# Kernel tuning notes

Hardware: AMD Instinct MI355X
Metric: run time of the kernel (lower is better)

The kernel has to match this reference:

```python
import jax, jax.numpy as jnp
import numpy as np

B, T, E, H, L, V = 16, 512, 512, 8, 4, 2048
HS = E // H  # head_size = n_embd // n_head
FF = 4 * E


def _ln(x, g, b):
    m = x.mean(-1, keepdims=True)
    v = ((x - m) ** 2).mean(-1, keepdims=True)
    return (x - m) * jax.lax.rsqrt(v + 1e-5) * g + b


def setup_inputs() -> dict:
    key = jax.random.key(0)
    ks = jax.random.split(key, 16)
    s = jnp.float32(0.02)
    return {
        "idx": jax.random.randint(ks[0], (B, T), 0, V),
        "tok_emb": jax.random.normal(ks[1], (V, E), jnp.float32) * s,
        "pos_emb": jax.random.normal(ks[2], (T, E), jnp.float32) * s,
        "Wq": jax.random.normal(ks[3], (L, E, E), jnp.float32) * s,
        "Wk": jax.random.normal(ks[4], (L, E, E), jnp.float32) * s,
        "Wv": jax.random.normal(ks[5], (L, E, E), jnp.float32) * s,
        "rel": jax.random.normal(ks[6], (L, 2 * T - 1, HS), jnp.float32) * s,
        "Wo": jax.random.normal(ks[7], (L, E, E), jnp.float32) * s,
        "bo": jnp.zeros((L, E), jnp.float32),
        "ln1_g": jnp.ones((L, E), jnp.float32),
        "ln1_b": jnp.zeros((L, E), jnp.float32),
        "W1": jax.random.normal(ks[8], (L, E, FF), jnp.float32) * s,
        "b1": jnp.zeros((L, FF), jnp.float32),
        "W2": jax.random.normal(ks[9], (L, FF, E), jnp.float32) * s,
        "b2": jnp.zeros((L, E), jnp.float32),
        "ln2_g": jnp.ones((L, E), jnp.float32),
        "ln2_b": jnp.zeros((L, E), jnp.float32),
        "lnf_g": jnp.ones((E,), jnp.float32),
        "lnf_b": jnp.zeros((E,), jnp.float32),
        "Wlm": jax.random.normal(ks[10], (E, V), jnp.float32) * s,
        "blm": jnp.zeros((V,), jnp.float32),
    }


def reference(idx, tok_emb, pos_emb, Wq, Wk, Wv, rel, Wo, bo, ln1_g, ln1_b,
              W1, b1, W2, b2, ln2_g, ln2_b, lnf_g, lnf_b, Wlm, blm):
    x = tok_emb[idx] + pos_emb[None, :T]  # (B,T,E)
    ri = jnp.arange(T)
    rel_idx = ri[:, None] - ri[None, :] + (T - 1)  # block_size == T
    causal = ri[:, None] >= ri[None, :]            # (T,T) lower-triangular
    scale = jnp.float32(1.0 / np.sqrt(HS))
    for l in range(L):
        h = _ln(x, ln1_g[l], ln1_b[l])
        # NOTE: torch code does .view(B, H, T, HS) on a (B, T, H*HS) tensor
        # (NOT a transpose) -- jnp.reshape matches row-major view semantics.
        q = (h @ Wq[l]).reshape(B, H, T, HS)
        k = (h @ Wk[l]).reshape(B, H, T, HS)
        v = (h @ Wv[l]).reshape(B, H, T, HS)
        re = rel[l][rel_idx]  # (T,T,HS)
        # rel scores: sum_d q[b,h,i,d]*re[i,j,d]; avoid the 5D intermediate
        scores = jnp.einsum('bhid,bhjd->bhij', q, k) * scale \
               + jnp.einsum('bhid,ijd->bhij', q, re)
        scores = jnp.where(causal, scores, -jnp.inf)
        att = jax.nn.softmax(scores, axis=-1)  # dropout disabled (eval)
        ctx = jnp.einsum('bhij,bhjd->bhid', att, v)
        ctx = jnp.swapaxes(ctx, 1, 2).reshape(B, T, H * HS)
        x = x + ctx @ Wo[l] + bo[l]
        h2 = _ln(x, ln2_g[l], ln2_b[l])
        x = x + jax.nn.relu(h2 @ W1[l] + b1[l]) @ W2[l] + b2[l]
    x = _ln(x, lnf_g, lnf_b)
    return x @ Wlm + blm  # logits (B,T,V)
```

## Files before the change

kernel.cpp:

```cpp
#include <hip/hip_runtime.h>
#include <hip/hip_bf16.h>
#include <stdint.h>

typedef __hip_bfloat16 bf16;
typedef __attribute__((ext_vector_type(8))) short bf16x8;
typedef __attribute__((ext_vector_type(8))) short short8;
typedef __attribute__((ext_vector_type(4))) float f32x4;

#define DEV __device__ __forceinline__

static constexpr int Bn = 16, Tn = 512, En = 512, Hn = 8, Ln = 4, Vn = 2048;
static constexpr int HSn = 64, FFn = 2048, Mn = Bn * Tn;
static constexpr int SQ = 1536;

DEV f32x4 mfma16(bf16x8 a, bf16x8 b, f32x4 c) {
  return __builtin_amdgcn_mfma_f32_16x16x32_bf16(a, b, c, 0, 0, 0);
}
DEV float b2f(bf16 x) { return __bfloat162float(x); }
DEV bf16 f2b(float x) { return __float2bfloat16(x); }
DEV short f2s(float x) { bf16 h = f2b(x); return reinterpret_cast<short&>(h); }

DEV void gload16(const void* g, void* l) {
  __builtin_amdgcn_global_load_lds(
      (const __attribute__((address_space(1))) void*)(uintptr_t)g,
      (__attribute__((address_space(3))) void*)(uint32_t)(uintptr_t)l, 16, 0, 0);
}

__global__ __launch_bounds__(256) void ktranspose(const float* __restrict__ in,
                                                  bf16* __restrict__ out, int R, int C,
                                                  long in_zs, long out_zs) {
  __shared__ float tile[32][33];
  int z = blockIdx.z;
  const float* inz = in + (size_t)z * in_zs;
  bf16* outz = out + (size_t)z * out_zs;
  int c0 = blockIdx.x * 32, r0 = blockIdx.y * 32;
  for (int k = 0; k < 32; k += 8)
    tile[threadIdx.y + k][threadIdx.x] =
        inz[(size_t)(r0 + threadIdx.y + k) * C + (c0 + threadIdx.x)];
  __syncthreads();
  for (int k = 0; k < 32; k += 8)
    outz[(size_t)(c0 + threadIdx.y + k) * R + (r0 + threadIdx.x)] =
        f2b(tile[threadIdx.x][threadIdx.y + k]);
}

__global__ __launch_bounds__(256) void kcast(const float* __restrict__ in,
                                             bf16* __restrict__ out, int n) {
  int i = blockIdx.x * 256 + threadIdx.x;
  if (i < n) out[i] = f2b(in[i]);
}

__global__ __launch_bounds__(256) void kembed(const int* __restrict__ idx,
                                              const float* __restrict__ tok,
                                              const float* __restrict__ pos,
                                              float* __restrict__ x) {
  int i = blockIdx.x * 256 + threadIdx.x;
  int e4 = (i & 127) * 4;
  int bt = i >> 7;
  int t = bt & (Tn - 1);
  f32x4 tv = *(const f32x4*)(tok + (size_t)idx[bt] * En + e4);
  f32x4 pv = *(const f32x4*)(pos + (size_t)t * En + e4);
  *(f32x4*)(x + (size_t)bt * En + e4) = tv + pv;
}

__global__ __launch_bounds__(256) void kln(const float* __restrict__ x,
                                           const float* __restrict__ g,
                                           const float* __restrict__ b,
                                           bf16* __restrict__ out) {
  int row = blockIdx.x * 4 + (threadIdx.x >> 6);
  int lane = threadIdx.x & 63;
  const float* xr = x + (size_t)row * En + lane * 8;
  f32x4 a0 = *(const f32x4*)xr;
  f32x4 a1 = *(const f32x4*)(xr + 4);
  float s = a0[0] + a0[1] + a0[2] + a0[3] + a1[0] + a1[1] + a1[2] + a1[3];
  for (int m = 1; m < 64; m <<= 1) s += __shfl_xor(s, m);
  float mean = s * (1.f / En);
  float s2 = 0.f;
  for (int j = 0; j < 4; j++) { float d0 = a0[j] - mean, d1 = a1[j] - mean; s2 += d0 * d0 + d1 * d1; }
  for (int m = 1; m < 64; m <<= 1) s2 += __shfl_xor(s2, m);
  float rstd = rsqrtf(s2 * (1.f / En) + 1e-5f);
  f32x4 g0 = *(const f32x4*)(g + lane * 8), g1 = *(const f32x4*)(g + lane * 8 + 4);
  f32x4 b0 = *(const f32x4*)(b + lane * 8), b1 = *(const f32x4*)(b + lane * 8 + 4);
  short8 ov;
  for (int j = 0; j < 4; j++) {
    ov[j] = f2s((a0[j] - mean) * rstd * g0[j] + b0[j]);
    ov[j + 4] = f2s((a1[j] - mean) * rstd * g1[j] + b1[j]);
  }
  *(short8*)(out + (size_t)row * En + lane * 8) = ov;
}

template <int BM, int BN, int TW, int DB, int SWZ, int NBIAS, int RELU, int MODE>
__global__ __launch_bounds__(TW) void kgemm(const bf16* __restrict__ A,
                                            const bf16* __restrict__ Bt,
                                            const float* __restrict__ bias,
                                            float* __restrict__ outf,
                                            bf16* __restrict__ outh, int Ndim, int K) {
  constexpr int NW = TW / 64;
  constexpr int WCN = NW / 2;
  constexpr int WM = BM / 2, WN = BN / WCN, MI = WM / 16, NI = WN / 16;
  constexpr int NB = DB ? 2 : 1;
  __shared__ bf16 As[NB][BM * 64];
  __shared__ bf16 Bs[NB][BN * 64];
  int t = threadIdx.x, lane = t & 63, w = t >> 6;
  int lr = lane & 15, lg = lane >> 4;
  int sx = lr & 7;
  int wr = w / WCN, wc = w % WCN;
  int bx, by;
  if (SWZ) {
    int id = blockIdx.x + gridDim.x * blockIdx.y;
    int xcd = id & 7, s = id >> 3;
    int gx = gridDim.x;
    by = xcd * 8 + s / gx;
    bx = s % gx;
  } else {
    bx = blockIdx.x; by = blockIdx.y;
  }
  int br = by * BM, bc = bx * BN;
  f32x4 acc[MI][NI] = {};
  int rl = lane >> 3, cb = (lane & 7) ^ rl;
  const bf16* Abase = A + (size_t)(br + w * (BM / NW) + rl) * K + cb * 8;
  const bf16* Bbase = Bt + (size_t)(bc + w * (BN / NW) + rl) * K + cb * 8;

  auto STAGE = [&](int buf, int kt) {
    for (int c = 0; c < BM / (8 * NW); c++)
      gload16(Abase + (size_t)(c * 8) * K + kt, &As[buf][(w * (BM / NW) + c * 8) * 64]);
    for (int c = 0; c < BN / (8 * NW); c++)
      gload16(Bbase + (size_t)(c * 8) * K + kt, &Bs[buf][(w * (BN / NW) + c * 8) * 64]);
  };
  auto COMPUTE = [&](int buf) {
    for (int kk = 0; kk < 2; kk++) {
      int gb = (kk * 4 + lg) ^ sx;
      bf16x8 af[MI], bfr[NI];
      for (int mi = 0; mi < MI; mi++)
        af[mi] = *(const bf16x8*)&As[buf][(wr * WM + mi * 16 + lr) * 64 + gb * 8];
      for (int ni = 0; ni < NI; ni++)
        bfr[ni] = *(const bf16x8*)&Bs[buf][(wc * WN + ni * 16 + lr) * 64 + gb * 8];
      for (int mi = 0; mi < MI; mi++)
        for (int ni = 0; ni < NI; ni++)
          acc[mi][ni] = mfma16(af[mi], bfr[ni], acc[mi][ni]);
    }
  };

  if (DB) {
    STAGE(0, 0);
    __syncthreads();
    int nt = K / 64;
    for (int t2 = 0; t2 < nt; t2++) {
      int cur = t2 & 1;
      if (t2 + 1 < nt) STAGE(cur ^ 1, (t2 + 1) * 64);
      COMPUTE(cur);
      __syncthreads();
    }
  } else {
    for (int kt = 0; kt < K; kt += 64) {
      __syncthreads();
      STAGE(0, kt);
      __syncthreads();
      COMPUTE(0);
    }
  }

  for (int mi = 0; mi < MI; mi++)
    for (int ni = 0; ni < NI; ni++)
      for (int r = 0; r < 4; r++) {
        int row = br + wr * WM + mi * 16 + lg * 4 + r;
        int col = bc + wc * WN + ni * 16 + lr;
        float val = acc[mi][ni][r];
        if (NBIAS) val += bias[col];
        if (RELU) val = fmaxf(val, 0.f);
        if (MODE == 1) outf[(size_t)row * Ndim + col] += val;
        else if (MODE == 2) outf[(size_t)row * Ndim + col] = val;
        else outh[(size_t)row * Ndim + col] = f2b(val);
      }
}

__global__ __launch_bounds__(512) void kattn(const bf16* __restrict__ qkv,
                                             const bf16* __restrict__ rel,
                                             bf16* __restrict__ ctx) {
  __shared__ bf16 Ks[128 * 64];
  __shared__ bf16 Vs[64 * 128];
  __shared__ bf16 Prel[8][16 * 81];
  __shared__ bf16 Ps[8][16 * 64];
  int pairp = blockIdx.x, bh = blockIdx.y;
  int b = bh >> 3, hh = bh & 7;
  int t = threadIdx.x, lane = t & 63, w = t >> 6;
  int wl = w & 3, wg = w >> 2;
  int lr = lane & 15, lg = lane >> 4;
  int sx = lr & 7;
  int rl8 = lane >> 3, cbk = (lane & 7) ^ rl8;
  const size_t headrow = (size_t)(b * Tn + hh * 64);
  bf16* prw = &Prel[w][0];
  bf16* psw = &Ps[w][0];
  int jp = t >> 3, db = (t & 7) * 8;

  int ia = pairp, ib = 7 - pairp;
  int myblk = wg ? ia : ib;
  int mylast = myblk * 64;
  int i0w = myblk * 64 + wl * 16;
  bf16x8 aq[2];
  {
    int t2 = i0w + lr;
    const bf16* qp = qkv + (headrow + (t2 >> 3)) * SQ + (t2 & 7) * 64;
    aq[0] = *(const bf16x8*)(qp + lg * 8);
    aq[1] = *(const bf16x8*)(qp + 32 + lg * 8);
  }
  f32x4 o[4] = {};
  float m_run = -3e38f, l_run = 0.f;
  int ntiles = (ib >> 1) + 1;

  auto SUBTILE = [&](int jb, bool diag, int su) {
    int njmax = diag ? wl : 3;
    int nmmin = diag ? 3 - wl : 0;
    __builtin_amdgcn_s_setprio(1);
    f32x4 sqk[4] = {};
    for (int nj = 0; nj <= njmax; nj++) {
      int row = su * 64 + nj * 16 + lr;
      bf16x8 kb0 = *(const bf16x8*)&Ks[row * 64 + ((lg ^ sx) * 8)];
      bf16x8 kb1 = *(const bf16x8*)&Ks[row * 64 + (((4 + lg) ^ sx) * 8)];
      sqk[nj] = mfma16(kb0, aq[0], sqk[nj]);
      sqk[nj] = mfma16(kb1, aq[1], sqk[nj]);
    }
    int base = i0w - jb + 448;
    for (int nm = nmmin; nm < 5; nm++) {
      int mrow = base + nm * 16 + lr;
      if (mrow > 1022) mrow = 1022;
      const bf16* rp = rel + (size_t)mrow * 64;
      f32x4 sr = {};
      sr = mfma16(aq[0], *(const bf16x8*)(rp + lg * 8), sr);
      sr = mfma16(aq[1], *(const bf16x8*)(rp + 32 + lg * 8), sr);
      for (int r = 0; r < 4; r++)
        prw[(lg * 4 + r) * 81 + nm * 16 + lr] = f2b(sr[r]);
    }
    __builtin_amdgcn_s_setprio(0);
    float sv[4][4];
    for (int nj = 0; nj < 4; nj++)
      for (int r = 0; r < 4; r++) sv[nj][r] = -3e38f;
    float mloc = -3e38f;
    for (int nj = 0; nj <= njmax; nj++)
      for (int r = 0; r < 4; r++) {
        int jj = nj * 16 + lg * 4 + r;
        float val = sqk[nj][r] * 0.125f + b2f(prw[lr * 81 + (lr - jj + 63)]);
        if (jb + jj > i0w + lr) val = -3e38f;
        sv[nj][r] = val;
        mloc = fmaxf(mloc, val);
      }
    mloc = fmaxf(mloc, __shfl_xor(mloc, 16));
    mloc = fmaxf(mloc, __shfl_xor(mloc, 32));
    float mnew = fmaxf(m_run, mloc);
    float corr = __expf(m_run - mnew);
    m_run = mnew;
    float lsum = 0.f;
    for (int nj = 0; nj < 4; nj++)
      for (int r = 0; r < 4; r++) {
        float p = __expf(sv[nj][r] - mnew);
        lsum += p;
        psw[lr * 64 + (((nj * 2 + (lg >> 1)) ^ sx) * 8) + (lg & 1) * 4 + r] = f2b(p);
      }
    lsum += __shfl_xor(lsum, 16);
    lsum += __shfl_xor(lsum, 32);
    l_run = l_run * corr + lsum;
    for (int r = 0; r < 4; r++) {
      float c = __shfl(corr, lg * 4 + r);
      for (int nd = 0; nd < 4; nd++) o[nd][r] *= c;
    }
    __builtin_amdgcn_s_setprio(1);
    bf16x8 ap0 = *(const bf16x8*)&psw[lr * 64 + ((lg ^ sx) * 8)];
    bf16x8 ap1 = *(const bf16x8*)&psw[lr * 64 + (((4 + lg) ^ sx) * 8)];
    for (int nd = 0; nd < 4; nd++) {
      int d = nd * 16 + lr;
      bf16x8 vb0 = *(const bf16x8*)&Vs[d * 128 + ((su * 8 + (lg ^ sx)) * 8)];
      bf16x8 vb1 = *(const bf16x8*)&Vs[d * 128 + ((su * 8 + ((4 + lg) ^ sx)) * 8)];
      o[nd] = mfma16(ap0, vb0, o[nd]);
      o[nd] = mfma16(ap1, vb1, o[nd]);
    }
    __builtin_amdgcn_s_setprio(0);
  };

  for (int jt = 0; jt < ntiles; jt++) {
    int jbase = jt * 128;
    bf16x8 vv[2];
#pragma unroll
    for (int u = 0; u < 2; u++) {
      int j0 = jbase + jp * 2 + u;
      vv[u] = *(const bf16x8*)(qkv + (headrow + (j0 >> 3)) * SQ + (j0 & 7) * 64 + 1024 + db);
    }
    __syncthreads();
#pragma unroll
    for (int c = 0; c < 2; c++) {
      int row = w * 16 + c * 8 + rl8;
      const bf16* src = qkv + (headrow + ((jbase + row) >> 3)) * SQ +
                        (row & 7) * 64 + 512 + cbk * 8;
      gload16(src, &Ks[(w * 16 + c * 8) * 64]);
    }
    {
      const short* pa = (const short*)&vv[0];
      const short* pb = (const short*)&vv[1];
      int j0 = jp * 2;
      int jblk = j0 >> 3, jin = j0 & 7;
#pragma unroll
      for (int u = 0; u < 8; u++) {
        int d = db + u;
        int idx = d * 128 + ((jblk ^ (d & 7)) * 8) + jin;
        uint32_t pk = (uint32_t)(uint16_t)pa[u] | ((uint32_t)(uint16_t)pb[u] << 16);
        *(uint32_t*)((short*)Vs + idx) = pk;
      }
    }
    __syncthreads();
#pragma unroll
    for (int su = 0; su < 2; su++) {
      int jb = jbase + su * 64;
      if (jb > ib * 64) break;
      if (jb <= mylast) SUBTILE(jb, jb == mylast, su);
    }
  }
  for (int r = 0; r < 4; r++) {
    float linv = 1.f / __shfl(l_run, lg * 4 + r);
    int row = i0w + lg * 4 + r;
    for (int nd = 0; nd < 4; nd++)
      ctx[((size_t)b * Tn + row) * En + hh * 64 + nd * 16 + lr] = f2b(o[nd][r] * linv);
  }
}

extern "C" void kernel_launch(void* const* d_in, const int* in_sizes, int n_in,
                              void* d_out, int out_size, void* d_ws, size_t ws_size,
                              hipStream_t stream) {
  (void)in_sizes; (void)n_in; (void)out_size; (void)ws_size;
  const int* idx = (const int*)d_in[0];
  const float* tok = (const float*)d_in[1];
  const float* pos = (const float*)d_in[2];
  const float* Wq = (const float*)d_in[3];
  const float* Wk = (const float*)d_in[4];
  const float* Wv = (const float*)d_in[5];
  const float* rel = (const float*)d_in[6];
  const float* Wo = (const float*)d_in[7];
  const float* bo = (const float*)d_in[8];
  const float* ln1_g = (const float*)d_in[9];
  const float* ln1_b = (const float*)d_in[10];
  const float* W1 = (const float*)d_in[11];
  const float* b1 = (const float*)d_in[12];
  const float* W2 = (const float*)d_in[13];
  const float* b2 = (const float*)d_in[14];
  const float* ln2_g = (const float*)d_in[15];
  const float* ln2_b = (const float*)d_in[16];
  const float* lnf_g = (const float*)d_in[17];
  const float* lnf_b = (const float*)d_in[18];
  const float* Wlm = (const float*)d_in[19];
  const float* blm = (const float*)d_in[20];

  char* ws = (char*)d_ws;
  float* x = (float*)(ws + 0);
  bf16* h = (bf16*)(ws + 16777216);
  bf16* qkv = (bf16*)(ws + 25165824);
  bf16* ctx = (bf16*)(ws + 50331648);
  bf16* ffn1 = qkv;
  bf16* wqkvT = (bf16*)(ws + 58720256);
  bf16* woT = wqkvT + (size_t)Ln * SQ * En;
  bf16* w1T = woT + (size_t)Ln * En * En;
  bf16* w2T = w1T + (size_t)Ln * En * FFn;
  bf16* wlmT = w2T + (size_t)Ln * FFn * En;
  bf16* relc = wlmT + (size_t)En * Vn;
  float* outf = (float*)d_out;

  dim3 tb(32, 8);
  ktranspose<<<dim3(16, 16, Ln), tb, 0, stream>>>(Wq, wqkvT, En, En, (long)En * En, (long)SQ * En);
  ktranspose<<<dim3(16, 16, Ln), tb, 0, stream>>>(Wk, wqkvT + 512 * 512, En, En, (long)En * En, (long)SQ * En);
  ktranspose<<<dim3(16, 16, Ln), tb, 0, stream>>>(Wv, wqkvT + 2 * 512 * 512, En, En, (long)En * En, (long)SQ * En);
  ktranspose<<<dim3(16, 16, Ln), tb, 0, stream>>>(Wo, woT, En, En, (long)En * En, (long)En * En);
  ktranspose<<<dim3(64, 16, Ln), tb, 0, stream>>>(W1, w1T, En, FFn, (long)En * FFn, (long)En * FFn);
  ktranspose<<<dim3(16, 64, Ln), tb, 0, stream>>>(W2, w2T, FFn, En, (long)FFn * En, (long)FFn * En);
  ktranspose<<<dim3(64, 16, 1), tb, 0, stream>>>(Wlm, wlmT, En, Vn, 0, 0);
  kcast<<<(Ln * (2 * Tn - 1) * HSn + 255) / 256, 256, 0, stream>>>(
      rel, relc, Ln * (2 * Tn - 1) * HSn);

  kembed<<<(Mn * En / 4) / 256, 256, 0, stream>>>(idx, tok, pos, x);

  for (int l = 0; l < Ln; l++) {
    kln<<<Mn / 4, 256, 0, stream>>>(x, ln1_g + (size_t)l * En, ln1_b + (size_t)l * En, h);
    kgemm<128, 128, 256, 0, 1, 0, 0, 0><<<dim3(12, 64), 256, 0, stream>>>(
        h, wqkvT + (size_t)l * SQ * En, nullptr, nullptr, qkv, SQ, En);
    kattn<<<dim3(4, 128), 512, 0, stream>>>(
        qkv, relc + (size_t)l * (2 * Tn - 1) * HSn, ctx);
    kgemm<128, 128, 512, 1, 1, 1, 0, 1><<<dim3(4, 64), 512, 0, stream>>>(
        ctx, woT + (size_t)l * En * En, bo + (size_t)l * En, x, nullptr, En, En);
    kln<<<Mn / 4, 256, 0, stream>>>(x, ln2_g + (size_t)l * En, ln2_b + (size_t)l * En, h);
    kgemm<128, 128, 256, 0, 1, 1, 1, 0><<<dim3(16, 64), 256, 0, stream>>>(
        h, w1T + (size_t)l * En * FFn, b1 + (size_t)l * FFn, nullptr, ffn1, FFn, En);
    kgemm<128, 128, 512, 1, 1, 1, 0, 1><<<dim3(4, 64), 512, 0, stream>>>(
        ffn1, w2T + (size_t)l * FFn * En, b2 + (size_t)l * En, x, nullptr, En, FFn);
  }
  kln<<<Mn / 4, 256, 0, stream>>>(x, lnf_g, lnf_b, h);
  kgemm<128, 128, 256, 0, 1, 1, 0, 2><<<dim3(16, 64), 256, 0, stream>>>(
      h, wlmT, blm, outf, nullptr, Vn, En);
}
```

Measured before the change: 645.8 us.

## Add 256x256 eight-wave GEMM for FFN1/LM head and tune attention LDS swizzle

Adds a new kgemm8 kernel with 256x256 output tiles, 8 waves, double-buffered direct-to-LDS loads staged in halves interleaved with MFMA phases, and an XCD-aware block remap. It replaces the FFN1 and LM-head GEMMs, aiming for more operand reuse per LDS byte and better L2 locality. The attention kernel also packs the bf16 P writes into 64-bit stores and changes the V tile swizzle so it depends on the thread lane bits, which should reduce LDS bank conflicts. The larger tile uses 128 KB of LDS and many accumulators, which limits occupancy to one block per CU.

Result: slower. 687.8 us (+6.5%).

```diff
diff --git a/kernel.cpp b/kernel.cpp
--- a/kernel.cpp
+++ b/kernel.cpp
@@ -19,6 +19,11 @@
 DEV float b2f(bf16 x) { return __bfloat162float(x); }
 DEV bf16 f2b(float x) { return __float2bfloat16(x); }
 DEV short f2s(float x) { bf16 h = f2b(x); return reinterpret_cast<short&>(h); }
+DEV uint32_t packbf(float a, float b) {
+  bf16 x = f2b(a), y = f2b(b);
+  return (uint32_t)reinterpret_cast<unsigned short&>(x) |
+         ((uint32_t)reinterpret_cast<unsigned short&>(y) << 16);
+}
 
 DEV void gload16(const void* g, void* l) {
   __builtin_amdgcn_global_load_lds(
@@ -173,6 +178,106 @@
       }
 }
 
+template <int NBIAS, int RELU, int MODE>
+__global__ __launch_bounds__(512) void kgemm8(const bf16* __restrict__ A,
+                                              const bf16* __restrict__ Bt,
+                                              const float* __restrict__ bias,
+                                              float* __restrict__ outf,
+                                              bf16* __restrict__ outh, int Ndim, int K) {
+  __shared__ bf16 As[2][256 * 64];
+  __shared__ bf16 Bs[2][256 * 64];
+  int t = threadIdx.x, lane = t & 63, w = t >> 6;
+  int lr = lane & 15, lg = lane >> 4;
+  int sx = lr & 7;
+  int wr = w >> 2, wc = w & 3;
+  int rl8 = lane >> 3, cb = (lane & 7) ^ rl8;
+  int id = blockIdx.x + gridDim.x * blockIdx.y;
+  int xcd = id & 7, s = id >> 3;
+  int by = xcd * 4 + (s >> 3), bx = s & 7;
+  int br = by * 256, bc = bx * 256;
+  f32x4 acc[8][4] = {};
+  const bf16* Abase = A + (size_t)(br + w * 16 + rl8) * K + cb * 8;
+  const bf16* Bbase = Bt + (size_t)(bc + w * 16 + rl8) * K + cb * 8;
+
+  auto STAGEH = [&](int hh, int buf, int kt) {
+    int half = hh & 1;
+    if (hh < 2) {
+      const bf16* g = Abase + (size_t)(half * 128) * K + kt;
+      bf16* l = &As[buf][(half * 128 + w * 16) * 64];
+      gload16(g, l);
+      gload16(g + (size_t)8 * K, l + 8 * 64);
+    } else {
+      const bf16* g = Bbase + (size_t)(half * 128) * K + kt;
+      bf16* l = &Bs[buf][(half * 128 + w * 16) * 64];
+      gload16(g, l);
+      gload16(g + (size_t)8 * K, l + 8 * 64);
+    }
+  };
+
+#define PHASE8(Q, P)                                                          \
+  do {                                                                        \
+    constexpr int mh = (Q) >> 1, nh = (Q) & 1;                                \
+    bf16x8 af[4][2], bfr[2][2];                                               \
+    _Pragma("unroll") for (int kk = 0; kk < 2; kk++) {                        \
+      int gb = (kk * 4 + lg) ^ sx;                                            \
+      _Pragma("unroll") for (int i = 0; i < 4; i++)                           \
+        af[i][kk] = *(const bf16x8*)&As[P][(wr * 128 + (mh * 4 + i) * 16 + lr) * 64 + gb * 8]; \
+      _Pragma("unroll") for (int j = 0; j < 2; j++)                           \
+        bfr[j][kk] = *(const bf16x8*)&Bs[P][(wc * 64 + (nh * 2 + j) * 16 + lr) * 64 + gb * 8]; \
+    }                                                                         \
+    __builtin_amdgcn_s_setprio(1);                                            \
+    _Pragma("unroll") for (int i = 0; i < 4; i++)                             \
+      _Pragma("unroll") for (int j = 0; j < 2; j++) {                         \
+        acc[mh * 4 + i][nh * 2 + j] =                                         \
+            mfma16(af[i][0], bfr[j][0], acc[mh * 4 + i][nh * 2 + j]);         \
+        acc[mh * 4 + i][nh * 2 + j] =                                         \
+            mfma16(af[i][1], bfr[j][1], acc[mh * 4 + i][nh * 2 + j]);         \
+      }                                                                       \
+    __builtin_amdgcn_s_setprio(0);                                            \
+  } while (0)
+
+  int nt = K / 64;
+  for (int hh = 0; hh < 4; hh++) STAGEH(hh, 0, 0);
+  STAGEH(0, 1, 64);
+  STAGEH(1, 1, 64);
+  asm volatile("s_waitcnt vmcnt(4)" ::: "memory");
+  asm volatile("s_barrier" ::: "memory");
+  for (int t2 = 0; t2 < nt; t2++) {
+    int p = t2 & 1;
+    if (t2 + 1 < nt) STAGEH(2, p ^ 1, (t2 + 1) * 64);
+    PHASE8(0, p);
+    if (t2 + 1 < nt) STAGEH(3, p ^ 1, (t2 + 1) * 64);
+    PHASE8(1, p);
+    PHASE8(2, p);
+    PHASE8(3, p);
+    asm volatile("s_barrier" ::: "memory");
+    if (t2 + 2 < nt) {
+      STAGEH(0, p, (t2 + 2) * 64);
+      STAGEH(1, p, (t2 + 2) * 64);
+      asm volatile("s_waitcnt vmcnt(4)" ::: "memory");
+      asm volatile("s_barrier" ::: "memory");
+    } else if (t2 + 1 < nt) {
+      asm volatile("s_waitcnt vmcnt(0)" ::: "memory");
+      asm volatile("s_barrier" ::: "memory");
+    }
+  }
+#undef PHASE8
+#pragma unroll
+  for (int mi = 0; mi < 8; mi++)
+#pragma unroll
+    for (int ni = 0; ni < 4; ni++)
+#pragma unroll
+      for (int r = 0; r < 4; r++) {
+        int row = br + wr * 128 + mi * 16 + lg * 4 + r;
+        int col = bc + wc * 64 + ni * 16 + lr;
+        float val = acc[mi][ni][r];
+        if (NBIAS) val += bias[col];
+        if (RELU) val = fmaxf(val, 0.f);
+        if (MODE == 2) outf[(size_t)row * Ndim + col] = val;
+        else outh[(size_t)row * Ndim + col] = f2b(val);
+      }
+}
+
 __global__ __launch_bounds__(512) void kattn(const bf16* __restrict__ qkv,
                                              const bf16* __restrict__ rel,
                                              bf16* __restrict__ ctx) {
@@ -190,7 +295,7 @@
   const size_t headrow = (size_t)(b * Tn + hh * 64);
   bf16* prw = &Prel[w][0];
   bf16* psw = &Ps[w][0];
-  int jp = t >> 3, db = (t & 7) * 8;
+  int jp = t >> 3, db = (t & 7) * 8, tf = t & 7;
 
   int ia = pairp, ib = 7 - pairp;
   int myblk = wg ? ia : ib;
@@ -249,12 +354,14 @@
     float corr = __expf(m_run - mnew);
     m_run = mnew;
     float lsum = 0.f;
-    for (int nj = 0; nj < 4; nj++)
-      for (int r = 0; r < 4; r++) {
-        float p = __expf(sv[nj][r] - mnew);
-        lsum += p;
-        psw[lr * 64 + (((nj * 2 + (lg >> 1)) ^ sx) * 8) + (lg & 1) * 4 + r] = f2b(p);
-      }
+#pragma unroll
+    for (int nj = 0; nj < 4; nj++) {
+      float p0 = __expf(sv[nj][0] - mnew), p1 = __expf(sv[nj][1] - mnew);
+      float p2 = __expf(sv[nj][2] - mnew), p3 = __expf(sv[nj][3] - mnew);
+      lsum += p0 + p1 + p2 + p3;
+      uint64_t pk = (uint64_t)packbf(p0, p1) | ((uint64_t)packbf(p2, p3) << 32);
+      *(uint64_t*)&psw[lr * 64 + (((nj * 2 + (lg >> 1)) ^ sx) * 8) + (lg & 1) * 4] = pk;
+    }
     lsum += __shfl_xor(lsum, 16);
     lsum += __shfl_xor(lsum, 32);
     l_run = l_run * corr + lsum;
@@ -265,10 +372,12 @@
     __builtin_amdgcn_s_setprio(1);
     bf16x8 ap0 = *(const bf16x8*)&psw[lr * 64 + ((lg ^ sx) * 8)];
     bf16x8 ap1 = *(const bf16x8*)&psw[lr * 64 + (((4 + lg) ^ sx) * 8)];
+#pragma unroll
     for (int nd = 0; nd < 4; nd++) {
       int d = nd * 16 + lr;
-      bf16x8 vb0 = *(const bf16x8*)&Vs[d * 128 + ((su * 8 + (lg ^ sx)) * 8)];
-      bf16x8 vb1 = *(const bf16x8*)&Vs[d * 128 + ((su * 8 + ((4 + lg) ^ sx)) * 8)];
+      int fr = sx ^ (nd * 2 + (lr >> 3));
+      bf16x8 vb0 = *(const bf16x8*)&Vs[d * 128 + ((su * 8 + (lg ^ fr)) * 8)];
+      bf16x8 vb1 = *(const bf16x8*)&Vs[d * 128 + ((su * 8 + ((4 + lg) ^ fr)) * 8)];
       o[nd] = mfma16(ap0, vb0, o[nd]);
       o[nd] = mfma16(ap1, vb1, o[nd]);
     }
@@ -299,7 +408,7 @@
 #pragma unroll
       for (int u = 0; u < 8; u++) {
         int d = db + u;
-        int idx = d * 128 + ((jblk ^ (d & 7)) * 8) + jin;
+        int idx = d * 128 + ((jblk ^ u ^ tf) * 8) + jin;
         uint32_t pk = (uint32_t)(uint16_t)pa[u] | ((uint32_t)(uint16_t)pb[u] << 16);
         *(uint32_t*)((short*)Vs + idx) = pk;
       }
@@ -382,12 +491,12 @@
     kgemm<128, 128, 512, 1, 1, 1, 0, 1><<<dim3(4, 64), 512, 0, stream>>>(
         ctx, woT + (size_t)l * En * En, bo + (size_t)l * En, x, nullptr, En, En);
     kln<<<Mn / 4, 256, 0, stream>>>(x, ln2_g + (size_t)l * En, ln2_b + (size_t)l * En, h);
-    kgemm<128, 128, 256, 0, 1, 1, 1, 0><<<dim3(16, 64), 256, 0, stream>>>(
+    kgemm8<1, 1, 0><<<dim3(8, 32), 512, 0, stream>>>(
         h, w1T + (size_t)l * En * FFn, b1 + (size_t)l * FFn, nullptr, ffn1, FFn, En);
     kgemm<128, 128, 512, 1, 1, 1, 0, 1><<<dim3(4, 64), 512, 0, stream>>>(
         ffn1, w2T + (size_t)l * FFn * En, b2 + (size_t)l * En, x, nullptr, En, FFn);
   }
   kln<<<Mn / 4, 256, 0, stream>>>(x, lnf_g, lnf_b, h);
-  kgemm<128, 128, 256, 0, 1, 1, 0, 2><<<dim3(16, 64), 256, 0, stream>>>(
+  kgemm8<1, 0, 2><<<dim3(8, 32), 512, 0, stream>>>(
       h, wlmT, blm, outf, nullptr, Vn, En);
 }
```
